# Kernel optimization log

Measured on AMD Instinct MI355X. Metric: run time of the kernel, lower is better.

## Reference

```python
import jax, jax.numpy as jnp
import numpy as np

D = 256; H = 4; HD = 64; NL = 12; MAXP = 16; DIM = 8; PDIM = 4; B = 128
EPS = 1e-5
SCALE = float(np.sqrt(HD))


def _ln(x, g, b):
    m = jnp.mean(x, -1, keepdims=True)
    v = jnp.mean((x - m) ** 2, -1, keepdims=True)
    return (x - m) * jax.lax.rsqrt(v + EPS) * g + b


def _mha(xq, xkv, Wqkv, bqkv, Wo, bo, causal):
    # Wqkv is the packed PyTorch in_proj_weight [3D, D]
    Bq, S, _ = xq.shape
    K = xkv.shape[1]
    q = (xq @ Wqkv[:D].T + bqkv[:D]).reshape(Bq, S, H, HD).transpose(0, 2, 1, 3)
    k = (xkv @ Wqkv[D:2 * D].T + bqkv[D:2 * D]).reshape(Bq, K, H, HD).transpose(0, 2, 1, 3)
    v = (xkv @ Wqkv[2 * D:].T + bqkv[2 * D:]).reshape(Bq, K, H, HD).transpose(0, 2, 1, 3)
    s = jnp.einsum('bhqd,bhkd->bhqk', q, k) / SCALE
    if causal:
        s = jnp.where(jnp.tril(jnp.ones((S, K), bool)), s, -jnp.inf)
    a = jax.nn.softmax(s, -1)
    o = jnp.einsum('bhqk,bhkd->bhqd', a, v).transpose(0, 2, 1, 3).reshape(Bq, S, D)
    return o @ Wo.T + bo


def _decode(tgt, mem, p):
    # post-LN TransformerDecoder (norm_first=False), dropout in eval mode
    x = tgt
    for l in range(NL):
        x = _ln(x + _mha(x, x, p['sa_Wqkv'][l], p['sa_bqkv'][l], p['sa_Wo'][l], p['sa_bo'][l], True), p['ln1_g'][l], p['ln1_b'][l])
        x = _ln(x + _mha(x, mem, p['ca_Wqkv'][l], p['ca_bqkv'][l], p['ca_Wo'][l], p['ca_bo'][l], False), p['ln2_g'][l], p['ln2_b'][l])
        h = jax.nn.relu(x @ p['lin1_W'][l].T + p['lin1_b'][l])
        x = _ln(x + h @ p['lin2_W'][l].T + p['lin2_b'][l], p['ln3_g'][l], p['ln3_b'][l])
    return x


def _forward(U_real, U_imag, tok_W, tok_b, pos_emb, sa_Wqkv, sa_bqkv, sa_Wo, sa_bo, ca_Wqkv, ca_bqkv, ca_Wo, ca_bo, lin1_W, lin1_b, lin2_W, lin2_b, ln1_g, ln1_b, ln2_g, ln2_b, ln3_g, ln3_b, out_W, out_b, param_low, param_high):
    p = dict(sa_Wqkv=sa_Wqkv, sa_bqkv=sa_bqkv, sa_Wo=sa_Wo, sa_bo=sa_bo,
             ca_Wqkv=ca_Wqkv, ca_bqkv=ca_bqkv, ca_Wo=ca_Wo, ca_bo=ca_bo,
             lin1_W=lin1_W, lin1_b=lin1_b, lin2_W=lin2_W, lin2_b=lin2_b,
             ln1_g=ln1_g, ln1_b=ln1_b, ln2_g=ln2_g, ln2_b=ln2_b, ln3_g=ln3_g, ln3_b=ln3_b)
    Bq = U_real.shape[0]
    vec = jnp.concatenate([U_real.reshape(Bq, -1), U_imag.reshape(Bq, -1)], -1)  # [B, 2*dim^2]
    src = vec @ tok_W.T + tok_b  # [B, D]
    mem = src[:, None, :]  # [B, 1, D] cross-attn memory
    seq = [src]
    for i in range(MAXP):
        tgt = jnp.stack(seq, 1) + pos_emb[:i + 1][None]  # [B, i+1, D]
        x = _decode(tgt, mem, p)
        seq.append(x[:, -1])
    logits = jnp.stack(seq[1:], 1)  # [B, MAXP, D]
    pn = jax.nn.sigmoid(logits @ out_W.T + out_b)  # [B, MAXP, PDIM]
    return param_low + (param_high - param_low) * pn


def setup_inputs() -> dict:
    key = jax.random.key(0)
    ks = jax.random.split(key, 16)
    def w(k, shape, s=0.02):
        return jax.random.normal(k, shape, dtype=jnp.float32) * s
    return {
        'U_real': jax.random.normal(ks[0], (B, DIM, DIM), dtype=jnp.float32),
        'U_imag': jax.random.normal(ks[1], (B, DIM, DIM), dtype=jnp.float32),
        'tok_W': w(ks[2], (D, 2 * DIM * DIM)), 'tok_b': jnp.zeros((D,), jnp.float32),
        'pos_emb': w(ks[3], (MAXP + 1, D)),
        'sa_Wqkv': w(ks[4], (NL, 3 * D, D)), 'sa_bqkv': jnp.zeros((NL, 3 * D), jnp.float32),
        'sa_Wo': w(ks[5], (NL, D, D)), 'sa_bo': jnp.zeros((NL, D), jnp.float32),
        'ca_Wqkv': w(ks[6], (NL, 3 * D, D)), 'ca_bqkv': jnp.zeros((NL, 3 * D), jnp.float32),
        'ca_Wo': w(ks[7], (NL, D, D)), 'ca_bo': jnp.zeros((NL, D), jnp.float32),
        'lin1_W': w(ks[8], (NL, 4 * D, D)), 'lin1_b': jnp.zeros((NL, 4 * D), jnp.float32),
        'lin2_W': w(ks[9], (NL, D, 4 * D)), 'lin2_b': jnp.zeros((NL, D), jnp.float32),
        'ln1_g': jnp.ones((NL, D), jnp.float32), 'ln1_b': jnp.zeros((NL, D), jnp.float32),
        'ln2_g': jnp.ones((NL, D), jnp.float32), 'ln2_b': jnp.zeros((NL, D), jnp.float32),
        'ln3_g': jnp.ones((NL, D), jnp.float32), 'ln3_b': jnp.zeros((NL, D), jnp.float32),
        'out_W': w(ks[10], (PDIM, D)), 'out_b': jnp.zeros((PDIM,), jnp.float32),
        'param_low': jnp.array([-1.0, 0.0, 0.0, 0.0], jnp.float32),
        'param_high': jnp.array([1.0, 1.0, 6.2832, 1.0], jnp.float32),
    }


def reference(U_real, U_imag, tok_W, tok_b, pos_emb, sa_Wqkv, sa_bqkv, sa_Wo, sa_bo, ca_Wqkv, ca_bqkv, ca_Wo, ca_bo, lin1_W, lin1_b, lin2_W, lin2_b, ln1_g, ln1_b, ln2_g, ln2_b, ln3_g, ln3_b, out_W, out_b, param_low, param_high):
    return _forward(U_real, U_imag, tok_W, tok_b, pos_emb, sa_Wqkv, sa_bqkv, sa_Wo, sa_bo, ca_Wqkv, ca_bqkv, ca_Wo, ca_bo, lin1_W, lin1_b, lin2_W, lin2_b, ln1_g, ln1_b, ln2_g, ln2_b, ln3_g, ln3_b, out_W, out_b, param_low, param_high)
```

## Files before the change

kernel.cpp:

```cpp
#include <hip/hip_runtime.h>
#include <hip/hip_bf16.h>


typedef __attribute__((ext_vector_type(8))) short short8;
typedef __attribute__((ext_vector_type(4))) float f32x4;

#define EPS_ 1e-5f

__device__ __forceinline__ unsigned short f2b(float x){
  union { float f; unsigned u; } c; c.f = x;
  unsigned r = (c.u + 0x7fffu + ((c.u >> 16) & 1u)) >> 16;
  return (unsigned short)r;
}
__device__ __forceinline__ float b2f(unsigned short u){
  union { unsigned u; float f; } c; c.u = ((unsigned)u) << 16;
  return c.f;
}
__device__ __forceinline__ unsigned long long pack4b(const f32x4 a){
  return (unsigned long long)f2b(a[0]) |
         ((unsigned long long)f2b(a[1]) << 16) |
         ((unsigned long long)f2b(a[2]) << 32) |
         ((unsigned long long)f2b(a[3]) << 48);
}
__device__ __forceinline__ unsigned long long pack2f(float a, float b){
  union { float f; unsigned u; } x, y; x.f = a; y.f = b;
  return (unsigned long long)x.u | ((unsigned long long)y.u << 32);
}
__device__ __forceinline__ float lo_f(unsigned long long v){
  union { unsigned u; float f; } c; c.u = (unsigned)v; return c.f;
}
__device__ __forceinline__ float hi_f(unsigned long long v){
  union { unsigned u; float f; } c; c.u = (unsigned)(v >> 32); return c.f;
}

#define AL(p)    __hip_atomic_load((p),  __ATOMIC_RELAXED, __HIP_MEMORY_SCOPE_AGENT)
#define AS(p,v)  __hip_atomic_store((p), (v), __ATOMIC_RELAXED, __HIP_MEMORY_SCOPE_AGENT)

__device__ __forceinline__ void gload16(const unsigned short* g, unsigned short* l){
  __builtin_amdgcn_global_load_lds(
      (const __attribute__((address_space(1))) unsigned int*)g,
      (__attribute__((address_space(3))) unsigned int*)l, 16, 0, 0);
}
#define WAIT_STG() do{ asm volatile("s_waitcnt vmcnt(0)" ::: "memory");      \
                       __builtin_amdgcn_sched_barrier(0); }while(0)
#define PIN_ORDER() __builtin_amdgcn_sched_barrier(0)

#define OFF_WQKV 0ull
#define OFF_WO   4718592ull
#define OFF_L1   6291456ull
#define OFF_L2   12582912ull
#define OFF_SRC  18874368ull
#define OFF_CC   19005440ull
#define OFF_KV   19791872ull
#define OFF_XH   44957696ull
#define OFF_ZA   45219840ull
#define OFF_ZB   45613056ull
#define OFF_FLG  46006272ull

__global__ void k_conv(const float* __restrict__ wqkv, const float* __restrict__ wo,
                       const float* __restrict__ l1, const float* __restrict__ l2,
                       unsigned short* __restrict__ dst){
  const long long nQ = 2359296, nW = 786432, nL1 = 3145728;
  const long long tot = 9437184;
  for (long long idx = (long long)blockIdx.x*256 + threadIdx.x; idx < tot;
       idx += (long long)gridDim.x*256){
    float v;
    long long i = idx;
    if (i < nQ){
      int l = (int)(i/196608); int r = (int)(i%196608);
      int h = r/49152; r %= 49152;
      int tile = r/4096; r %= 4096;
      int kc = r>>9; int lane = (r>>3)&63; int e = r&7;
      int p = tile>>2, q4 = tile&3;
      int n = p*256 + h*64 + q4*16 + (lane&15);
      int k = (lane>>4)*8 + kc*32 + e;
      v = wqkv[((long long)l*768 + n)*256 + k];
    } else if (i < nQ+nW){
      i -= nQ;
      int l = (int)(i/65536); int r = (int)(i%65536);
      int h = r/16384; r %= 16384;
      int tile = r/1024; r %= 1024;
      int kc = r>>9; int lane = (r>>3)&63; int e = r&7;
      int n = tile*16 + (lane&15);
      int k = h*64 + (lane>>4)*8 + kc*32 + e;
      v = wo[((long long)l*256 + n)*256 + k];
    } else if (i < nQ+nW+nL1){
      i -= nQ+nW;
      int l = (int)(i/262144); int r = (int)(i%262144);
      int h = r/65536; r %= 65536;
      int tile = r/4096; r %= 4096;
      int kc = r>>9; int lane = (r>>3)&63; int e = r&7;
      int n = h*256 + tile*16 + (lane&15);
      int k = (lane>>4)*8 + kc*32 + e;
      v = l1[((long long)l*1024 + n)*256 + k];
    } else {
      i -= nQ+nW+nL1;
      int l = (int)(i/262144); int r = (int)(i%262144);
      int h = r/65536; r %= 65536;
      int tile = r/4096; r %= 4096;
      int kc = r>>9; int lane = (r>>3)&63; int e = r&7;
      int n = tile*16 + (lane&15);
      int k = h*256 + (lane>>4)*8 + kc*32 + e;
      v = l2[((long long)l*256 + n)*1024 + k];
    }
    dst[idx] = f2b(v);
  }
}

__global__ void k_src(const float* __restrict__ U_real, const float* __restrict__ U_imag,
                      const float* __restrict__ tok_W, const float* __restrict__ tok_b,
                      const float* __restrict__ pos,
                      float* __restrict__ src, float* __restrict__ xh0){
  int b = blockIdx.x, n = threadIdx.x;
  const float* w = tok_W + n*128;
  const float* ur = U_real + b*64;
  const float* ui = U_imag + b*64;
  float acc = tok_b[n];
  #pragma unroll 8
  for (int k = 0; k < 64; ++k) acc += w[k]*ur[k];
  #pragma unroll 8
  for (int k = 0; k < 64; ++k) acc += w[64+k]*ui[k];
  src[b*256+n] = acc;
  xh0[b*256+n] = acc + pos[n];
}

__global__ void k_cc(const float* __restrict__ caW, const float* __restrict__ cab,
                     const float* __restrict__ caWo, const float* __restrict__ cabo,
                     const float* __restrict__ src, unsigned short* __restrict__ cc){
  int l = blockIdx.x >> 7, b = blockIdx.x & 127, t = threadIdx.x;
  __shared__ float v[256];
  const float* s = src + b*256;
  {
    const float* w = caW + ((long long)l*768 + 512 + t)*256;
    float a = cab[l*768 + 512 + t];
    #pragma unroll 8
    for (int k = 0; k < 256; ++k) a += w[k]*s[k];
    v[t] = a;
  }
  __syncthreads();
  {
    const float* w = caWo + ((long long)l*256 + t)*256;
    float a = cabo[l*256 + t];
    #pragma unroll 8
    for (int k = 0; k < 256; ++k) a += w[k]*v[k];
    cc[((long long)l*128 + b)*256 + t] = f2b(a);
  }
}

#define PUBW(FARR) do{                                                       \
  __syncthreads();                                                           \
  if (tid == 0) AS(FARR + l*4 + h, seq);                                     \
  if (tid < 3){                                                              \
    int ho = tid + (tid >= h ? 1 : 0);                                       \
    const int* fp = FARR + l*4 + ho;                                         \
    while (AL(fp) < seq) __builtin_amdgcn_s_sleep(1);                        \
  }                                                                          \
  __syncthreads();                                                           \
}while(0)

__global__ __launch_bounds__(512, 1) void k_main(
  const unsigned short* __restrict__ wqkv,
  const unsigned short* __restrict__ wo,
  const unsigned short* __restrict__ wl1,
  const unsigned short* __restrict__ wl2,
  const float* __restrict__ bqkv, const float* __restrict__ bo_,
  const float* __restrict__ bl1,  const float* __restrict__ bl2,
  const float* __restrict__ g1, const float* __restrict__ be1,
  const float* __restrict__ g2, const float* __restrict__ be2,
  const float* __restrict__ g3, const float* __restrict__ be3,
  const unsigned short* __restrict__ cc,
  const float* __restrict__ pos,
  const float* __restrict__ outW,
  const float* __restrict__ outb,
  const float* __restrict__ plow, const float* __restrict__ phigh,
  unsigned short* __restrict__ kvc,
  unsigned long long* __restrict__ xh,
  unsigned long long* __restrict__ zA,
  unsigned long long* __restrict__ zB,
  int* __restrict__ flags,
  float* __restrict__ out)
{
  __shared__ float xf[16][260];
  __shared__ float zf[16][260];
  __shared__ float yf[16][260];
  __shared__ unsigned short xb[16][264];
  __shared__ unsigned short hs[16][264];
  __shared__ unsigned short qs[16][72];
  __shared__ unsigned short os[16][72];
  __shared__ __align__(16) unsigned short stg[8][4096];

  const int tid  = threadIdx.x;
  const int w    = tid >> 6, lane = tid & 63;
  const int l    = blockIdx.x >> 2;
  const int h    = blockIdx.x & 3;
  const int mrow = lane & 15, kgrp = lane >> 4;

  int* fin = flags;
  int* fA  = flags + 384;
  int* fB  = flags + 432;

  const unsigned short* pQ  = wqkv + (size_t)(l*4 + h)*12*4096;
  const unsigned short* pWo = wo   + (size_t)(l*4 + h)*16*1024;
  const unsigned short* pL1 = wl1  + (size_t)(l*4 + h)*16*4096;
  const unsigned short* pL2 = wl2  + (size_t)(l*4 + h)*16*4096;
  unsigned short* sb = &stg[w][0];

  for (int t = 0; t < 16; ++t){
    for (int g = 0; g < 8; ++g){
      const int seq = t*8 + g + 1;

      {
        int need = (l == 0) ? t : (t+1);
        if (need > 0 && tid < 4){
          const int* fp = fin + (l*4 + tid)*8 + g;
          while (AL(fp) < need) __builtin_amdgcn_s_sleep(1);
        }
        __syncthreads();
        int row = tid >> 5, c8 = (tid & 31)*8;
        const unsigned long long* xp =
            xh + ((size_t)(l & 1)*8 + g)*2048 + (size_t)row*128 + (c8 >> 1);
        #pragma unroll
        for (int j = 0; j < 4; ++j){
          unsigned long long v = AL(xp + j);
          float f0 = lo_f(v), f1 = hi_f(v);
          xf[row][c8+2*j]   = f0;  xf[row][c8+2*j+1] = f1;
          xb[row][c8+2*j]   = f2b(f0);
          xb[row][c8+2*j+1] = f2b(f1);
        }
      }
      __syncthreads();

      {
        short8 a[8];
        #pragma unroll
        for (int kc = 0; kc < 8; ++kc)
          a[kc] = *(const short8*)&xb[mrow][kc*32 + kgrp*8];
        int nt = (w < 4) ? 2 : 1;
        for (int it = 0; it < nt; ++it){
          int tile = (it == 0) ? w : (8 + w);
          const unsigned short* src = pQ + (size_t)tile*4096;
          #pragma unroll
          for (int j = 0; j < 8; ++j)
            gload16(src + j*512 + lane*8, sb + j*512);
          WAIT_STG();
          f32x4 acc = {0,0,0,0};
          #pragma unroll
          for (int kc = 0; kc < 8; ++kc){
            short8 b0 = *(const short8*)(sb + kc*512 + lane*8);
            acc = __builtin_amdgcn_mfma_f32_16x16x32_bf16(a[kc], b0, acc, 0,0,0);
          }
          int p = tile >> 2, q4 = tile & 3;
          int n_l = q4*16 + mrow;
          float bias = bqkv[l*768 + p*256 + h*64 + n_l];
          #pragma unroll
          for (int r = 0; r < 4; ++r){
            int br = kgrp*4 + r;
            float v = acc[r] + bias;
            if (p == 0){
              qs[br][n_l] = f2b(v);
            } else {
              size_t kb = (((((size_t)l*4 + h)*8 + g)*16 + br)*16 + t)*128
                          + (p == 2 ? 64 : 0) + n_l;
              kvc[kb] = f2b(v);
            }
          }
          PIN_ORDER();
        }
      }
      __syncthreads();

      {
        int row = w*2 + (lane >> 5);
        int lid = lane & 31;
        float q0 = b2f(qs[row][lid*2]), q1 = b2f(qs[row][lid*2+1]);
        const unsigned short* base =
            kvc + (((((size_t)l*4 + h)*8 + g)*16 + row)*16)*128 + lid*2;
        float sv[16];
        #pragma unroll
        for (int j = 0; j < 16; ++j){
          if (j <= t){
            const unsigned short* kp = base + j*128;
            float p = q0*b2f(kp[0]) + q1*b2f(kp[1]);
            p += __shfl_xor(p, 1);
            p += __shfl_xor(p, 2);
            p += __shfl_xor(p, 4);
            p += __shfl_xor(p, 8);
            p += __shfl_xor(p, 16);
            sv[j] = p * 0.125f;
          } else sv[j] = -1e30f;
        }
        float mx = sv[0];
        #pragma unroll
        for (int j = 1; j < 16; ++j) mx = fmaxf(mx, sv[j]);
        float den = 0.f, e[16];
        #pragma unroll
        for (int j = 0; j < 16; ++j){ e[j] = __expf(sv[j]-mx); den += e[j]; }
        float rd = 1.f/den;
        float o0 = 0.f, o1 = 0.f;
        #pragma unroll
        for (int j = 0; j < 16; ++j){
          if (j <= t){
            const unsigned short* vp = base + j*128 + 64;
            o0 += e[j]*b2f(vp[0]);
            o1 += e[j]*b2f(vp[1]);
          }
        }
        os[row][lid*2]   = f2b(o0*rd);
        os[row][lid*2+1] = f2b(o1*rd);
      }
      __syncthreads();

      {
        short8 a2[2];
        #pragma unroll
        for (int kc = 0; kc < 2; ++kc)
          a2[kc] = *(const short8*)&os[mrow][kc*32 + kgrp*8];
        const unsigned short* src = pWo + (size_t)(w*2)*1024;
        #pragma unroll
        for (int j = 0; j < 4; ++j)
          gload16(src + j*512 + lane*8, sb + j*512);
        WAIT_STG();
        #pragma unroll
        for (int u2 = 0; u2 < 2; ++u2){
          int n_g = (w*2+u2)*16 + mrow;
          f32x4 acc = {0,0,0,0};
          #pragma unroll
          for (int kc = 0; kc < 2; ++kc){
            short8 b0 = *(const short8*)(sb + u2*1024 + kc*512 + lane*8);
            acc = __builtin_amdgcn_mfma_f32_16x16x32_bf16(a2[kc], b0, acc, 0,0,0);
          }
          AS(zA + ((size_t)(l*4 + h)*256 + n_g)*4 + kgrp, pack4b(acc));
        }
        PIN_ORDER();
      }
      PUBW(fA);

      {
        int col = tid & 255, rq2 = tid >> 8;
        float a8[8] = {0,0,0,0,0,0,0,0};
        #pragma unroll
        for (int s4 = 0; s4 < 4; ++s4){
          const unsigned long long* bp = zA + ((size_t)(l*4 + s4)*256 + col)*4 + rq2*2;
          #pragma unroll
          for (int q = 0; q < 2; ++q){
            unsigned long long v = AL(bp + q);
            a8[q*4+0] += b2f((unsigned short)v);
            a8[q*4+1] += b2f((unsigned short)(v >> 16));
            a8[q*4+2] += b2f((unsigned short)(v >> 32));
            a8[q*4+3] += b2f((unsigned short)(v >> 48));
          }
        }
        float bias = bo_[l*256 + col];
        #pragma unroll
        for (int r = 0; r < 8; ++r){
          int row = rq2*8 + r;
          zf[row][col] = a8[r] + bias + xf[row][col];
        }
      }
      __syncthreads();

      {
        int row = tid >> 5, c8 = (tid & 31)*8;
        float tt[8];
        #pragma unroll
        for (int k = 0; k < 8; ++k) tt[k] = zf[row][c8+k];
        float sm = 0, sq = 0;
        #pragma unroll
        for (int k = 0; k < 8; ++k){ sm += tt[k]; sq += tt[k]*tt[k]; }
        sm += __shfl_xor(sm,1);  sq += __shfl_xor(sq,1);
        sm += __shfl_xor(sm,2);  sq += __shfl_xor(sq,2);
        sm += __shfl_xor(sm,4);  sq += __shfl_xor(sq,4);
        sm += __shfl_xor(sm,8);  sq += __shfl_xor(sq,8);
        sm += __shfl_xor(sm,16); sq += __shfl_xor(sq,16);
        float mean = sm*(1.f/256), var = sq*(1.f/256) - mean*mean;
        float rs = rsqrtf(var + EPS_);
        const float* g1p = g1 + l*256 + c8;
        const float* b1p = be1 + l*256 + c8;
        const unsigned short* ccp = cc + ((size_t)l*128 + g*16 + row)*256 + c8;
        #pragma unroll
        for (int k = 0; k < 8; ++k)
          tt[k] = (tt[k]-mean)*rs*g1p[k] + b1p[k] + b2f(ccp[k]);
        sm = 0; sq = 0;
        #pragma unroll
        for (int k = 0; k < 8; ++k){ sm += tt[k]; sq += tt[k]*tt[k]; }
        sm += __shfl_xor(sm,1);  sq += __shfl_xor(sq,1);
        sm += __shfl_xor(sm,2);  sq += __shfl_xor(sq,2);
        sm += __shfl_xor(sm,4);  sq += __shfl_xor(sq,4);
        sm += __shfl_xor(sm,8);  sq += __shfl_xor(sq,8);
        sm += __shfl_xor(sm,16); sq += __shfl_xor(sq,16);
        mean = sm*(1.f/256); var = sq*(1.f/256) - mean*mean;
        rs = rsqrtf(var + EPS_);
        const float* g2p = g2 + l*256 + c8;
        const float* b2p = be2 + l*256 + c8;
        #pragma unroll
        for (int k = 0; k < 8; ++k){
          float y = (tt[k]-mean)*rs*g2p[k] + b2p[k];
          yf[row][c8+k] = y;
          xb[row][c8+k] = f2b(y);
        }
      }
      __syncthreads();

      {
        short8 a[8];
        #pragma unroll
        for (int kc = 0; kc < 8; ++kc)
          a[kc] = *(const short8*)&xb[mrow][kc*32 + kgrp*8];
        for (int it = 0; it < 2; ++it){
          int tile = w*2 + it;
          const unsigned short* src = pL1 + (size_t)tile*4096;
          #pragma unroll
          for (int j = 0; j < 8; ++j)
            gload16(src + j*512 + lane*8, sb + j*512);
          WAIT_STG();
          f32x4 acc = {0,0,0,0};
          #pragma unroll
          for (int kc = 0; kc < 8; ++kc){
            short8 b0 = *(const short8*)(sb + kc*512 + lane*8);
            acc = __builtin_amdgcn_mfma_f32_16x16x32_bf16(a[kc], b0, acc, 0,0,0);
          }
          int n_sl = tile*16 + mrow;
          float bias = bl1[l*1024 + h*256 + n_sl];
          #pragma unroll
          for (int r = 0; r < 4; ++r){
            float hv = acc[r] + bias;
            hs[kgrp*4 + r][n_sl] = f2b(hv > 0.f ? hv : 0.f);
          }
          PIN_ORDER();
        }
      }
      __syncthreads();

      {
        short8 ah[8];
        #pragma unroll
        for (int kc = 0; kc < 8; ++kc)
          ah[kc] = *(const short8*)&hs[mrow][kc*32 + kgrp*8];
        for (int it = 0; it < 2; ++it){
          int tile = w*2 + it;
          const unsigned short* src = pL2 + (size_t)tile*4096;
          #pragma unroll
          for (int j = 0; j < 8; ++j)
            gload16(src + j*512 + lane*8, sb + j*512);
          WAIT_STG();
          f32x4 acc = {0,0,0,0};
          #pragma unroll
          for (int kc = 0; kc < 8; ++kc){
            short8 b0 = *(const short8*)(sb + kc*512 + lane*8);
            acc = __builtin_amdgcn_mfma_f32_16x16x32_bf16(ah[kc], b0, acc, 0,0,0);
          }
          int n_g = tile*16 + mrow;
          AS(zB + ((size_t)(l*4 + h)*256 + n_g)*4 + kgrp, pack4b(acc));
          PIN_ORDER();
        }
      }
      PUBW(fB);

      {
        int col = tid & 255, rq2 = tid >> 8;
        float a8[8] = {0,0,0,0,0,0,0,0};
        #pragma unroll
        for (int s4 = 0; s4 < 4; ++s4){
          const unsigned long long* bp = zB + ((size_t)(l*4 + s4)*256 + col)*4 + rq2*2;
          #pragma unroll
          for (int q = 0; q < 2; ++q){
            unsigned long long v = AL(bp + q);
            a8[q*4+0] += b2f((unsigned short)v);
            a8[q*4+1] += b2f((unsigned short)(v >> 16));
            a8[q*4+2] += b2f((unsigned short)(v >> 32));
            a8[q*4+3] += b2f((unsigned short)(v >> 48));
          }
        }
        float bias = bl2[l*256 + col];
        #pragma unroll
        for (int r = 0; r < 8; ++r){
          int row = rq2*8 + r;
          zf[row][col] = a8[r] + bias + yf[row][col];
        }
      }
      __syncthreads();

      {
        int row = tid >> 5, c8 = (tid & 31)*8;
        float tt[8];
        #pragma unroll
        for (int k = 0; k < 8; ++k) tt[k] = zf[row][c8+k];
        float sm = 0, sq = 0;
        #pragma unroll
        for (int k = 0; k < 8; ++k){ sm += tt[k]; sq += tt[k]*tt[k]; }
        sm += __shfl_xor(sm,1);  sq += __shfl_xor(sq,1);
        sm += __shfl_xor(sm,2);  sq += __shfl_xor(sq,2);
        sm += __shfl_xor(sm,4);  sq += __shfl_xor(sq,4);
        sm += __shfl_xor(sm,8);  sq += __shfl_xor(sq,8);
        sm += __shfl_xor(sm,16); sq += __shfl_xor(sq,16);
        float mean = sm*(1.f/256), var = sq*(1.f/256) - mean*mean;
        float rs = rsqrtf(var + EPS_);
        const float* g3p = g3 + l*256 + c8;
        const float* b3p = be3 + l*256 + c8;
        float xn[8];
        #pragma unroll
        for (int k = 0; k < 8; ++k)
          xn[k] = (tt[k]-mean)*rs*g3p[k] + b3p[k];

        float pr[4] = {0,0,0,0};
        const bool doHead = (l == 11) && (h == 0);
        if (doHead){
          #pragma unroll
          for (int p = 0; p < 4; ++p){
            float a = 0.f;
            #pragma unroll
            for (int k = 0; k < 8; ++k) a += xn[k]*outW[p*256 + c8 + k];
            a += __shfl_xor(a,1); a += __shfl_xor(a,2);
            a += __shfl_xor(a,4); a += __shfl_xor(a,8);
            a += __shfl_xor(a,16);
            pr[p] = a;
          }
        }
        if (l == 11 && t < 15){
          const float* pp = pos + (t+1)*256 + c8;
          #pragma unroll
          for (int k = 0; k < 8; ++k) xn[k] += pp[k];
        }
        const bool last = (l == 11) && (t == 15);
        if (!last && ((c8 >> 6) == h)){
          unsigned long long* xp =
              xh + ((size_t)((l+1) & 1)*8 + g)*2048 + (size_t)row*128 + (c8 >> 1);
          #pragma unroll
          for (int j = 0; j < 4; ++j)
            AS(xp + j, pack2f(xn[2*j], xn[2*j+1]));
        }
        __syncthreads();
        if (!last && tid == 0)
          AS(fin + (((l+1) % 12)*4 + h)*8 + g, t+1);
        if (doHead && ((tid & 31) == 0)){
          int gr = g*16 + row;
          #pragma unroll
          for (int p = 0; p < 4; ++p){
            float v2 = pr[p] + outb[p];
            float sg = 1.f/(1.f + __expf(-v2));
            out[((size_t)gr*16 + t)*4 + p] = plow[p] + (phigh[p]-plow[p])*sg;
          }
        }
      }
    }
  }
}

extern "C" void kernel_launch(void* const* d_in, const int* in_sizes, int n_in,
                              void* d_out, int out_size, void* d_ws, size_t ws_size,
                              hipStream_t stream) {
  const float* U_real = (const float*)d_in[0];
  const float* U_imag = (const float*)d_in[1];
  const float* tok_W  = (const float*)d_in[2];
  const float* tok_b  = (const float*)d_in[3];
  const float* pos    = (const float*)d_in[4];
  const float* saW    = (const float*)d_in[5];
  const float* sab    = (const float*)d_in[6];
  const float* saWo   = (const float*)d_in[7];
  const float* sabo   = (const float*)d_in[8];
  const float* caW    = (const float*)d_in[9];
  const float* cab    = (const float*)d_in[10];
  const float* caWo   = (const float*)d_in[11];
  const float* cabo   = (const float*)d_in[12];
  const float* l1W    = (const float*)d_in[13];
  const float* l1b    = (const float*)d_in[14];
  const float* l2W    = (const float*)d_in[15];
  const float* l2b    = (const float*)d_in[16];
  const float* g1     = (const float*)d_in[17];
  const float* be1    = (const float*)d_in[18];
  const float* g2     = (const float*)d_in[19];
  const float* be2    = (const float*)d_in[20];
  const float* g3     = (const float*)d_in[21];
  const float* be3    = (const float*)d_in[22];
  const float* outW   = (const float*)d_in[23];
  const float* outb   = (const float*)d_in[24];
  const float* plow   = (const float*)d_in[25];
  const float* phigh  = (const float*)d_in[26];

  char* ws = (char*)d_ws;
  unsigned short* wb        = (unsigned short*)(ws + OFF_WQKV);
  float* srcb               = (float*)(ws + OFF_SRC);
  unsigned short* ccb       = (unsigned short*)(ws + OFF_CC);
  unsigned short* kvc       = (unsigned short*)(ws + OFF_KV);
  unsigned long long* xhb   = (unsigned long long*)(ws + OFF_XH);
  unsigned long long* zAb   = (unsigned long long*)(ws + OFF_ZA);
  unsigned long long* zBb   = (unsigned long long*)(ws + OFF_ZB);
  int* flags                = (int*)(ws + OFF_FLG);

  (void)hipMemsetAsync(ws + OFF_FLG, 0, 4096, stream);
  k_conv<<<dim3(4608), dim3(256), 0, stream>>>(saW, saWo, l1W, l2W, wb);
  k_src<<<dim3(128), dim3(256), 0, stream>>>(U_real, U_imag, tok_W, tok_b, pos,
                                             srcb, (float*)xhb);
  k_cc<<<dim3(1536), dim3(256), 0, stream>>>(caW, cab, caWo, cabo, srcb, ccb);
  k_main<<<dim3(48), dim3(512), 0, stream>>>(
      wb,
      (unsigned short*)(ws + OFF_WO),
      (unsigned short*)(ws + OFF_L1),
      (unsigned short*)(ws + OFF_L2),
      sab, sabo, l1b, l2b,
      g1, be1, g2, be2, g3, be3,
      ccb, pos, outW, outb, plow, phigh,
      kvc, xhb, zAb, zBb, flags, (float*)d_out);
}
```

Baseline: 4.527 ms.

## Prefetch next weight tile into LDS staging across GEMM phases

```diff
diff --git a/kernel.cpp b/kernel.cpp
--- a/kernel.cpp
+++ b/kernel.cpp
@@ -43,7 +43,8 @@
 }
 #define WAIT_STG() do{ asm volatile("s_waitcnt vmcnt(0)" ::: "memory");      \
                        __builtin_amdgcn_sched_barrier(0); }while(0)
-#define PIN_ORDER() __builtin_amdgcn_sched_barrier(0)
+#define LGKM0()    do{ asm volatile("s_waitcnt lgkmcnt(0)" ::: "memory");    \
+                       __builtin_amdgcn_sched_barrier(0); }while(0)
 
 #define OFF_WQKV 0ull
 #define OFF_WO   4718592ull
@@ -187,7 +188,8 @@
   __shared__ unsigned short hs[16][264];
   __shared__ unsigned short qs[16][72];
   __shared__ unsigned short os[16][72];
-  __shared__ __align__(16) unsigned short stg[8][4096];
+  __shared__ __align__(16) unsigned short stgA[8][4096];
+  __shared__ __align__(16) unsigned short stgB[8][1024];
 
   const int tid  = threadIdx.x;
   const int w    = tid >> 6, lane = tid & 63;
@@ -203,12 +205,20 @@
   const unsigned short* pWo = wo   + (size_t)(l*4 + h)*16*1024;
   const unsigned short* pL1 = wl1  + (size_t)(l*4 + h)*16*4096;
   const unsigned short* pL2 = wl2  + (size_t)(l*4 + h)*16*4096;
-  unsigned short* sb = &stg[w][0];
+  unsigned short* sbA = &stgA[w][0];
+  unsigned short* sbB = &stgB[w][0];
 
   for (int t = 0; t < 16; ++t){
     for (int g = 0; g < 8; ++g){
       const int seq = t*8 + g + 1;
 
+      {
+        LGKM0();
+        const unsigned short* src = pQ + (size_t)w*4096;
+        #pragma unroll
+        for (int j = 0; j < 8; ++j)
+          gload16(src + j*512 + lane*8, sbA + j*512);
+      }
       {
         int need = (l == 0) ? t : (t+1);
         if (need > 0 && tid < 4){
@@ -238,16 +248,25 @@
         int nt = (w < 4) ? 2 : 1;
         for (int it = 0; it < nt; ++it){
           int tile = (it == 0) ? w : (8 + w);
-          const unsigned short* src = pQ + (size_t)tile*4096;
-          #pragma unroll
-          for (int j = 0; j < 8; ++j)
-            gload16(src + j*512 + lane*8, sb + j*512);
           WAIT_STG();
           f32x4 acc = {0,0,0,0};
           #pragma unroll
           for (int kc = 0; kc < 8; ++kc){
-            short8 b0 = *(const short8*)(sb + kc*512 + lane*8);
+            short8 b0 = *(const short8*)(sbA + kc*512 + lane*8);
             acc = __builtin_amdgcn_mfma_f32_16x16x32_bf16(a[kc], b0, acc, 0,0,0);
+          }
+          if (it == 0 && nt == 2){
+            LGKM0();
+            const unsigned short* src2 = pQ + (size_t)(8 + w)*4096;
+            #pragma unroll
+            for (int j = 0; j < 8; ++j)
+              gload16(src2 + j*512 + lane*8, sbA + j*512);
+          }
+          if (it == nt-1){
+            const unsigned short* srcW = pWo + (size_t)(w*2)*1024;
+            #pragma unroll
+            for (int j = 0; j < 2; ++j)
+              gload16(srcW + j*512 + lane*8, sbB + j*512);
           }
           int p = tile >> 2, q4 = tile & 3;
           int n_l = q4*16 + mrow;
@@ -264,7 +283,6 @@
               kvc[kb] = f2b(v);
             }
           }
-          PIN_ORDER();
         }
       }
       __syncthreads();
@@ -315,23 +333,29 @@
         #pragma unroll
         for (int kc = 0; kc < 2; ++kc)
           a2[kc] = *(const short8*)&os[mrow][kc*32 + kgrp*8];
-        const unsigned short* src = pWo + (size_t)(w*2)*1024;
-        #pragma unroll
-        for (int j = 0; j < 4; ++j)
-          gload16(src + j*512 + lane*8, sb + j*512);
-        WAIT_STG();
-        #pragma unroll
         for (int u2 = 0; u2 < 2; ++u2){
+          WAIT_STG();
+          f32x4 acc = {0,0,0,0};
+          #pragma unroll
+          for (int kc = 0; kc < 2; ++kc){
+            short8 b0 = *(const short8*)(sbB + kc*512 + lane*8);
+            acc = __builtin_amdgcn_mfma_f32_16x16x32_bf16(a2[kc], b0, acc, 0,0,0);
+          }
+          if (u2 == 0){
+            LGKM0();
+            const unsigned short* srcW = pWo + (size_t)(w*2+1)*1024;
+            #pragma unroll
+            for (int j = 0; j < 2; ++j)
+              gload16(srcW + j*512 + lane*8, sbB + j*512);
+          } else {
+            const unsigned short* srcL = pL1 + (size_t)(w*2)*4096;
+            #pragma unroll
+            for (int j = 0; j < 8; ++j)
+              gload16(srcL + j*512 + lane*8, sbA + j*512);
+          }
           int n_g = (w*2+u2)*16 + mrow;
-          f32x4 acc = {0,0,0,0};
-          #pragma unroll
-          for (int kc = 0; kc < 2; ++kc){
-            short8 b0 = *(const short8*)(sb + u2*1024 + kc*512 + lane*8);
-            acc = __builtin_amdgcn_mfma_f32_16x16x32_bf16(a2[kc], b0, acc, 0,0,0);
-          }
           AS(zA + ((size_t)(l*4 + h)*256 + n_g)*4 + kgrp, pack4b(acc));
         }
-        PIN_ORDER();
       }
       PUBW(fA);
 
@@ -408,16 +432,24 @@
           a[kc] = *(const short8*)&xb[mrow][kc*32 + kgrp*8];
         for (int it = 0; it < 2; ++it){
           int tile = w*2 + it;
-          const unsigned short* src = pL1 + (size_t)tile*4096;
-          #pragma unroll
-          for (int j = 0; j < 8; ++j)
-            gload16(src + j*512 + lane*8, sb + j*512);
           WAIT_STG();
           f32x4 acc = {0,0,0,0};
           #pragma unroll
           for (int kc = 0; kc < 8; ++kc){
-            short8 b0 = *(const short8*)(sb + kc*512 + lane*8);
+            short8 b0 = *(const short8*)(sbA + kc*512 + lane*8);
             acc = __builtin_amdgcn_mfma_f32_16x16x32_bf16(a[kc], b0, acc, 0,0,0);
+          }
+          LGKM0();
+          if (it == 0){
+            const unsigned short* srcL = pL1 + (size_t)(w*2+1)*4096;
+            #pragma unroll
+            for (int j = 0; j < 8; ++j)
+              gload16(srcL + j*512 + lane*8, sbA + j*512);
+          } else {
+            const unsigned short* srcL = pL2 + (size_t)(w*2)*4096;
+            #pragma unroll
+            for (int j = 0; j < 8; ++j)
+              gload16(srcL + j*512 + lane*8, sbA + j*512);
           }
           int n_sl = tile*16 + mrow;
           float bias = bl1[l*1024 + h*256 + n_sl];
@@ -426,7 +458,6 @@
             float hv = acc[r] + bias;
             hs[kgrp*4 + r][n_sl] = f2b(hv > 0.f ? hv : 0.f);
           }
-          PIN_ORDER();
         }
       }
       __syncthreads();
@@ -438,20 +469,22 @@
           ah[kc] = *(const short8*)&hs[mrow][kc*32 + kgrp*8];
         for (int it = 0; it < 2; ++it){
           int tile = w*2 + it;
-          const unsigned short* src = pL2 + (size_t)tile*4096;
-          #pragma unroll
-          for (int j = 0; j < 8; ++j)
-            gload16(src + j*512 + lane*8, sb + j*512);
           WAIT_STG();
           f32x4 acc = {0,0,0,0};
           #pragma unroll
           for (int kc = 0; kc < 8; ++kc){
-            short8 b0 = *(const short8*)(sb + kc*512 + lane*8);
+            short8 b0 = *(const short8*)(sbA + kc*512 + lane*8);
             acc = __builtin_amdgcn_mfma_f32_16x16x32_bf16(ah[kc], b0, acc, 0,0,0);
+          }
+          if (it == 0){
+            LGKM0();
+            const unsigned short* srcL = pL2 + (size_t)(w*2+1)*4096;
+            #pragma unroll
+            for (int j = 0; j < 8; ++j)
+              gload16(srcL + j*512 + lane*8, sbA + j*512);
           }
           int n_g = tile*16 + mrow;
           AS(zB + ((size_t)(l*4 + h)*256 + n_g)*4 + kgrp, pack4b(acc));
-          PIN_ORDER();
         }
       }
       PUBW(fB);
```

Result: slower. 4.620 ms (+2.0%).

## Defer FFN-output reduction and final layernorm to the next layer's blocks

Applied to the files above, without the earlier changes.

```diff
diff --git a/kernel.cpp b/kernel.cpp
--- a/kernel.cpp
+++ b/kernel.cpp
@@ -22,16 +22,6 @@
          ((unsigned long long)f2b(a[2]) << 32) |
          ((unsigned long long)f2b(a[3]) << 48);
 }
-__device__ __forceinline__ unsigned long long pack2f(float a, float b){
-  union { float f; unsigned u; } x, y; x.f = a; y.f = b;
-  return (unsigned long long)x.u | ((unsigned long long)y.u << 32);
-}
-__device__ __forceinline__ float lo_f(unsigned long long v){
-  union { unsigned u; float f; } c; c.u = (unsigned)v; return c.f;
-}
-__device__ __forceinline__ float hi_f(unsigned long long v){
-  union { unsigned u; float f; } c; c.u = (unsigned)(v >> 32); return c.f;
-}
 
 #define AL(p)    __hip_atomic_load((p),  __ATOMIC_RELAXED, __HIP_MEMORY_SCOPE_AGENT)
 #define AS(p,v)  __hip_atomic_store((p), (v), __ATOMIC_RELAXED, __HIP_MEMORY_SCOPE_AGENT)
@@ -49,13 +39,14 @@
 #define OFF_WO   4718592ull
 #define OFF_L1   6291456ull
 #define OFF_L2   12582912ull
-#define OFF_SRC  18874368ull
-#define OFF_CC   19005440ull
-#define OFF_KV   19791872ull
-#define OFF_XH   44957696ull
-#define OFF_ZA   45219840ull
-#define OFF_ZB   45613056ull
-#define OFF_FLG  46006272ull
+#define OFF_CC   18874368ull
+#define OFF_KV   19660800ull
+#define OFF_ZA   43253760ull
+#define OFF_ZB   44040192ull
+#define OFF_ZB11 44761088ull
+#define OFF_PRM  45285376ull
+#define OFF_SRC  45350912ull
+#define OFF_FLG  45481984ull
 
 __global__ void k_conv(const float* __restrict__ wqkv, const float* __restrict__ wo,
                        const float* __restrict__ l1, const float* __restrict__ l2,
@@ -110,7 +101,7 @@
 __global__ void k_src(const float* __restrict__ U_real, const float* __restrict__ U_imag,
                       const float* __restrict__ tok_W, const float* __restrict__ tok_b,
                       const float* __restrict__ pos,
-                      float* __restrict__ src, float* __restrict__ xh0){
+                      float* __restrict__ src, unsigned short* __restrict__ prime){
   int b = blockIdx.x, n = threadIdx.x;
   const float* w = tok_W + n*128;
   const float* ur = U_real + b*64;
@@ -121,7 +112,7 @@
   #pragma unroll 8
   for (int k = 0; k < 64; ++k) acc += w[64+k]*ui[k];
   src[b*256+n] = acc;
-  xh0[b*256+n] = acc + pos[n];
+  prime[b*256+n] = f2b(acc + pos[n]);
 }
 
 __global__ void k_cc(const float* __restrict__ caW, const float* __restrict__ cab,
@@ -174,9 +165,10 @@
   const float* __restrict__ outb,
   const float* __restrict__ plow, const float* __restrict__ phigh,
   unsigned short* __restrict__ kvc,
-  unsigned long long* __restrict__ xh,
   unsigned long long* __restrict__ zA,
-  unsigned long long* __restrict__ zB,
+  unsigned long long* __restrict__ zBa,
+  unsigned long long* __restrict__ zB11,
+  const unsigned short* __restrict__ prime,
   int* __restrict__ flags,
   float* __restrict__ out)
 {
@@ -186,6 +178,8 @@
   __shared__ unsigned short xb[16][264];
   __shared__ unsigned short hs[16][264];
   __shared__ unsigned short qs[16][72];
+  __shared__ unsigned short ks[16][72];
+  __shared__ unsigned short vs[16][72];
   __shared__ unsigned short os[16][72];
   __shared__ __align__(16) unsigned short stg[8][4096];
 
@@ -197,13 +191,13 @@
 
   int* fin = flags;
   int* fA  = flags + 384;
-  int* fB  = flags + 432;
 
   const unsigned short* pQ  = wqkv + (size_t)(l*4 + h)*12*4096;
   const unsigned short* pWo = wo   + (size_t)(l*4 + h)*16*1024;
   const unsigned short* pL1 = wl1  + (size_t)(l*4 + h)*16*4096;
   const unsigned short* pL2 = wl2  + (size_t)(l*4 + h)*16*4096;
   unsigned short* sb = &stg[w][0];
+  const int lprev = (l == 0) ? 11 : (l-1);
 
   for (int t = 0; t < 16; ++t){
     for (int g = 0; g < 8; ++g){
@@ -216,16 +210,97 @@
           while (AL(fp) < need) __builtin_amdgcn_s_sleep(1);
         }
         __syncthreads();
+      }
+      if (l == 0 && t == 0){
         int row = tid >> 5, c8 = (tid & 31)*8;
-        const unsigned long long* xp =
-            xh + ((size_t)(l & 1)*8 + g)*2048 + (size_t)row*128 + (c8 >> 1);
-        #pragma unroll
-        for (int j = 0; j < 4; ++j){
-          unsigned long long v = AL(xp + j);
-          float f0 = lo_f(v), f1 = hi_f(v);
-          xf[row][c8+2*j]   = f0;  xf[row][c8+2*j+1] = f1;
-          xb[row][c8+2*j]   = f2b(f0);
-          xb[row][c8+2*j+1] = f2b(f1);
+        short8 v = *(const short8*)(prime + (size_t)(g*16 + row)*256 + c8);
+        #pragma unroll
+        for (int k = 0; k < 8; ++k){
+          unsigned short us = (unsigned short)((short*)&v)[k];
+          xf[row][c8+k] = b2f(us);
+          xb[row][c8+k] = us;
+        }
+      } else {
+        const int tp = (l == 0) ? (t-1) : t;
+        {
+          int col = tid & 255, rq2 = tid >> 8;
+          float a8[8] = {0,0,0,0,0,0,0,0};
+          #pragma unroll
+          for (int s4 = 0; s4 < 4; ++s4){
+            const unsigned long long* bp;
+            if (lprev == 11)
+              bp = zB11 + ((size_t)(s4*16 + (tp&1)*8 + g)*256 + col)*4 + rq2*2;
+            else
+              bp = zBa + (((size_t)(lprev*4 + s4)*2 + ((tp*8+g)&1))*256 + col)*4 + rq2*2;
+            #pragma unroll
+            for (int q = 0; q < 2; ++q){
+              unsigned long long v = AL(bp + q);
+              a8[q*4+0] += b2f((unsigned short)v);
+              a8[q*4+1] += b2f((unsigned short)(v >> 16));
+              a8[q*4+2] += b2f((unsigned short)(v >> 32));
+              a8[q*4+3] += b2f((unsigned short)(v >> 48));
+            }
+          }
+          float bias = bl2[lprev*256 + col];
+          #pragma unroll
+          for (int r = 0; r < 8; ++r)
+            zf[rq2*8 + r][col] = a8[r] + bias;
+        }
+        __syncthreads();
+        {
+          int row = tid >> 5, c8 = (tid & 31)*8;
+          float tt[8];
+          #pragma unroll
+          for (int k = 0; k < 8; ++k) tt[k] = zf[row][c8+k];
+          float sm = 0, sq = 0;
+          #pragma unroll
+          for (int k = 0; k < 8; ++k){ sm += tt[k]; sq += tt[k]*tt[k]; }
+          sm += __shfl_xor(sm,1);  sq += __shfl_xor(sq,1);
+          sm += __shfl_xor(sm,2);  sq += __shfl_xor(sq,2);
+          sm += __shfl_xor(sm,4);  sq += __shfl_xor(sq,4);
+          sm += __shfl_xor(sm,8);  sq += __shfl_xor(sq,8);
+          sm += __shfl_xor(sm,16); sq += __shfl_xor(sq,16);
+          float mean = sm*(1.f/256), var = sq*(1.f/256) - mean*mean;
+          float rs = rsqrtf(var + EPS_);
+          const float* g3p = g3 + lprev*256 + c8;
+          const float* b3p = be3 + lprev*256 + c8;
+          float xn[8];
+          #pragma unroll
+          for (int k = 0; k < 8; ++k)
+            xn[k] = (tt[k]-mean)*rs*g3p[k] + b3p[k];
+          if (l == 0){
+            if (h == 0){
+              float pr[4];
+              #pragma unroll
+              for (int p = 0; p < 4; ++p){
+                float a = 0.f;
+                #pragma unroll
+                for (int k = 0; k < 8; ++k) a += xn[k]*outW[p*256 + c8 + k];
+                a += __shfl_xor(a,1); a += __shfl_xor(a,2);
+                a += __shfl_xor(a,4); a += __shfl_xor(a,8);
+                a += __shfl_xor(a,16);
+                pr[p] = a;
+              }
+              if ((tid & 31) == 0){
+                int gr = g*16 + row;
+                #pragma unroll
+                for (int p = 0; p < 4; ++p){
+                  float v2 = pr[p] + outb[p];
+                  float sg = 1.f/(1.f + __expf(-v2));
+                  out[((size_t)gr*16 + (t-1))*4 + p] =
+                      plow[p] + (phigh[p]-plow[p])*sg;
+                }
+              }
+            }
+            const float* pp = pos + t*256 + c8;
+            #pragma unroll
+            for (int k = 0; k < 8; ++k) xn[k] += pp[k];
+          }
+          #pragma unroll
+          for (int k = 0; k < 8; ++k){
+            xf[row][c8+k] = xn[k];
+            xb[row][c8+k] = f2b(xn[k]);
+          }
         }
       }
       __syncthreads();
@@ -239,6 +314,9 @@
         for (int it = 0; it < nt; ++it){
           int tile = (it == 0) ? w : (8 + w);
           const unsigned short* src = pQ + (size_t)tile*4096;
+          LGKM_GUARD:;
+          asm volatile("s_waitcnt lgkmcnt(0)" ::: "memory");
+          __builtin_amdgcn_sched_barrier(0);
           #pragma unroll
           for (int j = 0; j < 8; ++j)
             gload16(src + j*512 + lane*8, sb + j*512);
@@ -259,9 +337,13 @@
             if (p == 0){
               qs[br][n_l] = f2b(v);
             } else {
-              size_t kb = (((((size_t)l*4 + h)*8 + g)*16 + br)*16 + t)*128
-                          + (p == 2 ? 64 : 0) + n_l;
-              kvc[kb] = f2b(v);
+              unsigned short bv = f2b(v);
+              if (p == 1) ks[br][n_l] = bv; else vs[br][n_l] = bv;
+              if (t < 15){
+                size_t kb = (((((size_t)l*4 + h)*8 + g)*16 + br)*15 + t)*128
+                            + (p == 2 ? 64 : 0) + n_l;
+                kvc[kb] = bv;
+              }
             }
           }
           PIN_ORDER();
@@ -274,13 +356,19 @@
         int lid = lane & 31;
         float q0 = b2f(qs[row][lid*2]), q1 = b2f(qs[row][lid*2+1]);
         const unsigned short* base =
-            kvc + (((((size_t)l*4 + h)*8 + g)*16 + row)*16)*128 + lid*2;
+            kvc + (((((size_t)l*4 + h)*8 + g)*16 + row)*15)*128 + lid*2;
         float sv[16];
         #pragma unroll
         for (int j = 0; j < 16; ++j){
           if (j <= t){
-            const unsigned short* kp = base + j*128;
-            float p = q0*b2f(kp[0]) + q1*b2f(kp[1]);
+            float k0, k1;
+            if (j < t){
+              const unsigned short* kp = base + j*128;
+              k0 = b2f(kp[0]); k1 = b2f(kp[1]);
+            } else {
+              k0 = b2f(ks[row][lid*2]); k1 = b2f(ks[row][lid*2+1]);
+            }
+            float p = q0*k0 + q1*k1;
             p += __shfl_xor(p, 1);
             p += __shfl_xor(p, 2);
             p += __shfl_xor(p, 4);
@@ -300,9 +388,15 @@
         #pragma unroll
         for (int j = 0; j < 16; ++j){
           if (j <= t){
-            const unsigned short* vp = base + j*128 + 64;
-            o0 += e[j]*b2f(vp[0]);
-            o1 += e[j]*b2f(vp[1]);
+            float v0, v1;
+            if (j < t){
+              const unsigned short* vp = base + j*128 + 64;
+              v0 = b2f(vp[0]); v1 = b2f(vp[1]);
+            } else {
+              v0 = b2f(vs[row][lid*2]); v1 = b2f(vs[row][lid*2+1]);
+            }
+            o0 += e[j]*v0;
+            o1 += e[j]*v1;
           }
         }
         os[row][lid*2]   = f2b(o0*rd);
@@ -316,10 +410,13 @@
         for (int kc = 0; kc < 2; ++kc)
           a2[kc] = *(const short8*)&os[mrow][kc*32 + kgrp*8];
         const unsigned short* src = pWo + (size_t)(w*2)*1024;
+        asm volatile("s_waitcnt lgkmcnt(0)" ::: "memory");
+        __builtin_amdgcn_sched_barrier(0);
         #pragma unroll
         for (int j = 0; j < 4; ++j)
           gload16(src + j*512 + lane*8, sb + j*512);
         WAIT_STG();
+        int slot = (t*8 + g) & 1;
         #pragma unroll
         for (int u2 = 0; u2 < 2; ++u2){
           int n_g = (w*2+u2)*16 + mrow;
@@ -329,7 +426,7 @@
             short8 b0 = *(const short8*)(sb + u2*1024 + kc*512 + lane*8);
             acc = __builtin_amdgcn_mfma_f32_16x16x32_bf16(a2[kc], b0, acc, 0,0,0);
           }
-          AS(zA + ((size_t)(l*4 + h)*256 + n_g)*4 + kgrp, pack4b(acc));
+          AS(zA + (((size_t)(l*4 + h)*2 + slot)*256 + n_g)*4 + kgrp, pack4b(acc));
         }
         PIN_ORDER();
       }
@@ -337,10 +434,12 @@
 
       {
         int col = tid & 255, rq2 = tid >> 8;
+        int slot = (t*8 + g) & 1;
         float a8[8] = {0,0,0,0,0,0,0,0};
         #pragma unroll
         for (int s4 = 0; s4 < 4; ++s4){
-          const unsigned long long* bp = zA + ((size_t)(l*4 + s4)*256 + col)*4 + rq2*2;
+          const unsigned long long* bp =
+              zA + (((size_t)(l*4 + s4)*2 + slot)*256 + col)*4 + rq2*2;
           #pragma unroll
           for (int q = 0; q < 2; ++q){
             unsigned long long v = AL(bp + q);
@@ -409,6 +508,8 @@
         for (int it = 0; it < 2; ++it){
           int tile = w*2 + it;
           const unsigned short* src = pL1 + (size_t)tile*4096;
+          asm volatile("s_waitcnt lgkmcnt(0)" ::: "memory");
+          __builtin_amdgcn_sched_barrier(0);
           #pragma unroll
           for (int j = 0; j < 8; ++j)
             gload16(src + j*512 + lane*8, sb + j*512);
@@ -427,6 +528,14 @@
             hs[kgrp*4 + r][n_sl] = f2b(hv > 0.f ? hv : 0.f);
           }
           PIN_ORDER();
+        }
+      }
+      if (l < 11){
+        int up = t*8 + g - 2;
+        if (up >= 0 && tid < 4){
+          int tU = up >> 3, gU = up & 7;
+          const int* fp = fin + (((l+2) % 12)*4 + tid)*8 + gU;
+          while (AL(fp) < tU+1) __builtin_amdgcn_s_sleep(1);
         }
       }
       __syncthreads();
@@ -439,6 +548,8 @@
         for (int it = 0; it < 2; ++it){
           int tile = w*2 + it;
           const unsigned short* src = pL2 + (size_t)tile*4096;
+          asm volatile("s_waitcnt lgkmcnt(0)" ::: "memory");
+          __builtin_amdgcn_sched_barrier(0);
           #pragma unroll
           for (int j = 0; j < 8; ++j)
             gload16(src + j*512 + lane*8, sb + j*512);
@@ -450,18 +561,40 @@
             acc = __builtin_amdgcn_mfma_f32_16x16x32_bf16(ah[kc], b0, acc, 0,0,0);
           }
           int n_g = tile*16 + mrow;
-          AS(zB + ((size_t)(l*4 + h)*256 + n_g)*4 + kgrp, pack4b(acc));
+          int rb = kgrp*4;
+          acc[0] += 0.25f*yf[rb+0][n_g];
+          acc[1] += 0.25f*yf[rb+1][n_g];
+          acc[2] += 0.25f*yf[rb+2][n_g];
+          acc[3] += 0.25f*yf[rb+3][n_g];
+          if (l < 11){
+            int slot = (t*8 + g) & 1;
+            AS(zBa + (((size_t)(l*4 + h)*2 + slot)*256 + n_g)*4 + kgrp, pack4b(acc));
+          } else {
+            AS(zB11 + ((size_t)(h*16 + (t&1)*8 + g)*256 + n_g)*4 + kgrp, pack4b(acc));
+          }
           PIN_ORDER();
         }
       }
-      PUBW(fB);
-
+      __syncthreads();
+      if (tid == 0)
+        AS(fin + (((l+1) % 12)*4 + h)*8 + g, t+1);
+    }
+  }
+
+  if (l == 11 && h == 0){
+    for (int g2 = 0; g2 < 8; ++g2){
+      if (tid < 4){
+        const int* fp = fin + (0*4 + tid)*8 + g2;
+        while (AL(fp) < 16) __builtin_amdgcn_s_sleep(1);
+      }
+      __syncthreads();
       {
         int col = tid & 255, rq2 = tid >> 8;
         float a8[8] = {0,0,0,0,0,0,0,0};
         #pragma unroll
         for (int s4 = 0; s4 < 4; ++s4){
-          const unsigned long long* bp = zB + ((size_t)(l*4 + s4)*256 + col)*4 + rq2*2;
+          const unsigned long long* bp =
+              zB11 + ((size_t)(s4*16 + 8 + g2)*256 + col)*4 + rq2*2;
           #pragma unroll
           for (int q = 0; q < 2; ++q){
             unsigned long long v = AL(bp + q);
@@ -471,15 +604,12 @@
             a8[q*4+3] += b2f((unsigned short)(v >> 48));
           }
         }
-        float bias = bl2[l*256 + col];
-        #pragma unroll
-        for (int r = 0; r < 8; ++r){
-          int row = rq2*8 + r;
-          zf[row][col] = a8[r] + bias + yf[row][col];
-        }
-      }
-      __syncthreads();
-
+        float bias = bl2[11*256 + col];
+        #pragma unroll
+        for (int r = 0; r < 8; ++r)
+          zf[rq2*8 + r][col] = a8[r] + bias;
+      }
+      __syncthreads();
       {
         int row = tid >> 5, c8 = (tid & 31)*8;
         float tt[8];
@@ -495,53 +625,32 @@
         sm += __shfl_xor(sm,16); sq += __shfl_xor(sq,16);
         float mean = sm*(1.f/256), var = sq*(1.f/256) - mean*mean;
         float rs = rsqrtf(var + EPS_);
-        const float* g3p = g3 + l*256 + c8;
-        const float* b3p = be3 + l*256 + c8;
         float xn[8];
         #pragma unroll
         for (int k = 0; k < 8; ++k)
-          xn[k] = (tt[k]-mean)*rs*g3p[k] + b3p[k];
-
-        float pr[4] = {0,0,0,0};
-        const bool doHead = (l == 11) && (h == 0);
-        if (doHead){
-          #pragma unroll
-          for (int p = 0; p < 4; ++p){
-            float a = 0.f;
-            #pragma unroll
-            for (int k = 0; k < 8; ++k) a += xn[k]*outW[p*256 + c8 + k];
-            a += __shfl_xor(a,1); a += __shfl_xor(a,2);
-            a += __shfl_xor(a,4); a += __shfl_xor(a,8);
-            a += __shfl_xor(a,16);
-            pr[p] = a;
-          }
-        }
-        if (l == 11 && t < 15){
-          const float* pp = pos + (t+1)*256 + c8;
-          #pragma unroll
-          for (int k = 0; k < 8; ++k) xn[k] += pp[k];
-        }
-        const bool last = (l == 11) && (t == 15);
-        if (!last && ((c8 >> 6) == h)){
-          unsigned long long* xp =
-              xh + ((size_t)((l+1) & 1)*8 + g)*2048 + (size_t)row*128 + (c8 >> 1);
-          #pragma unroll
-          for (int j = 0; j < 4; ++j)
-            AS(xp + j, pack2f(xn[2*j], xn[2*j+1]));
-        }
-        __syncthreads();
-        if (!last && tid == 0)
-          AS(fin + (((l+1) % 12)*4 + h)*8 + g, t+1);
-        if (doHead && ((tid & 31) == 0)){
-          int gr = g*16 + row;
+          xn[k] = (tt[k]-mean)*rs*g3[11*256 + c8 + k] + be3[11*256 + c8 + k];
+        float pr[4];
+        #pragma unroll
+        for (int p = 0; p < 4; ++p){
+          float a = 0.f;
+          #pragma unroll
+          for (int k = 0; k < 8; ++k) a += xn[k]*outW[p*256 + c8 + k];
+          a += __shfl_xor(a,1); a += __shfl_xor(a,2);
+          a += __shfl_xor(a,4); a += __shfl_xor(a,8);
+          a += __shfl_xor(a,16);
+          pr[p] = a;
+        }
+        if ((tid & 31) == 0){
+          int gr = g2*16 + row;
           #pragma unroll
           for (int p = 0; p < 4; ++p){
             float v2 = pr[p] + outb[p];
             float sg = 1.f/(1.f + __expf(-v2));
-            out[((size_t)gr*16 + t)*4 + p] = plow[p] + (phigh[p]-plow[p])*sg;
-          }
-        }
-      }
+            out[((size_t)gr*16 + 15)*4 + p] = plow[p] + (phigh[p]-plow[p])*sg;
+          }
+        }
+      }
+      __syncthreads();
     }
   }
 }
@@ -579,18 +688,19 @@
 
   char* ws = (char*)d_ws;
   unsigned short* wb        = (unsigned short*)(ws + OFF_WQKV);
-  float* srcb               = (float*)(ws + OFF_SRC);
   unsigned short* ccb       = (unsigned short*)(ws + OFF_CC);
   unsigned short* kvc       = (unsigned short*)(ws + OFF_KV);
-  unsigned long long* xhb   = (unsigned long long*)(ws + OFF_XH);
   unsigned long long* zAb   = (unsigned long long*)(ws + OFF_ZA);
-  unsigned long long* zBb   = (unsigned long long*)(ws + OFF_ZB);
+  unsigned long long* zBab  = (unsigned long long*)(ws + OFF_ZB);
+  unsigned long long* zB11b = (unsigned long long*)(ws + OFF_ZB11);
+  unsigned short* prm       = (unsigned short*)(ws + OFF_PRM);
+  float* srcb               = (float*)(ws + OFF_SRC);
   int* flags                = (int*)(ws + OFF_FLG);
 
   (void)hipMemsetAsync(ws + OFF_FLG, 0, 4096, stream);
   k_conv<<<dim3(4608), dim3(256), 0, stream>>>(saW, saWo, l1W, l2W, wb);
   k_src<<<dim3(128), dim3(256), 0, stream>>>(U_real, U_imag, tok_W, tok_b, pos,
-                                             srcb, (float*)xhb);
+                                             srcb, prm);
   k_cc<<<dim3(1536), dim3(256), 0, stream>>>(caW, cab, caWo, cabo, srcb, ccb);
   k_main<<<dim3(48), dim3(512), 0, stream>>>(
       wb,
@@ -600,5 +710,5 @@
       sab, sabo, l1b, l2b,
       g1, be1, g2, be2, g3, be3,
       ccb, pos, outW, outb, plow, phigh,
-      kvc, xhb, zAb, zBb, flags, (float*)d_out);
-}
+      kvc, zAb, zBab, zB11b, prm, flags, (float*)d_out);
+}
```

Result: slower. 4.638 ms (+2.5%).
